# Performance work log

Hardware: AMD Instinct MI355X
Metric: run time of the kernel (lower is better)

## Reference

```python
import jax, jax.numpy as jnp
import numpy as np

NUM_HEADS = 8
FOCUSING_FACTOR = 3
EPS = 1e-6


def _focus(x, f):
    # focusing: x**f, renormalized to keep the original L2 norm per token
    n = jnp.linalg.norm(x, axis=-1, keepdims=True)
    xp = x ** f
    return xp / jnp.linalg.norm(xp, axis=-1, keepdims=True) * n


def _split_heads(x, h):
    # b n (h c) -> (b h) n c
    b, n, C = x.shape
    return x.reshape(b, n, h, C // h).transpose(0, 2, 1, 3).reshape(b * h, n, C // h)


def setup_inputs() -> dict:
    key = jax.random.key(0)
    ks = jax.random.split(key, 9)
    B, Nq, Nkv, C = 8, 4096, 4096, 512
    query = jax.random.normal(ks[0], (B, Nq, C), jnp.float32)
    key_in = jax.random.normal(ks[1], (B, Nkv, C), jnp.float32)
    value = jax.random.normal(ks[2], (B, Nkv, C), jnp.float32)
    Wq = jax.random.normal(ks[3], (C, C), jnp.float32) * 0.02
    Wk = jax.random.normal(ks[4], (C, C), jnp.float32) * 0.02
    Wv = jax.random.normal(ks[5], (C, C), jnp.float32) * 0.02
    Wp = jax.random.normal(ks[6], (C, C), jnp.float32) * 0.02
    bp = jnp.zeros((C,), jnp.float32)
    scale = jax.random.normal(ks[7], (1, 1, C), jnp.float32) * 0.02
    return {"query": query, "key_in": key_in, "value": value,
            "Wq": Wq, "Wk": Wk, "Wv": Wv, "Wp": Wp, "bp": bp,
            "scale": scale, "H": 64, "W": 64}


def reference(query, key_in, value, Wq, Wk, Wv, Wp, bp, scale, H, W):
    B, N, C = query.shape
    h = NUM_HEADS
    # projections (qkv_bias=False)
    q = jax.nn.relu(query @ Wq) + EPS
    k = jax.nn.relu(key_in @ Wk) + EPS
    v = value @ Wv
    s = jax.nn.softplus(scale)  # [1,1,C]
    q = q / s
    k = k / s
    q = _focus(q, FOCUSING_FACTOR)
    k = _focus(k, FOCUSING_FACTOR)
    q = _split_heads(q, h)  # [(B h), N, c]
    k = _split_heads(k, h)
    v = _split_heads(v, h)
    # z-normalizer: 1 / (q . sum_j k_j)
    z = 1.0 / (jnp.einsum('bic,bc->bi', q, k.sum(axis=1)) + EPS)
    # O(n) kv-aggregation path (i*j*(c+d) > c*d*(i+j) for these shapes)
    kv = jnp.einsum('bjc,bjd->bcd', k, v)
    x = jnp.einsum('bic,bcd,bi->bid', q, kv, z)
    # (b h) n c -> b n (h c)
    x = x.reshape(B, h, N, C // h).transpose(0, 2, 1, 3).reshape(B, N, C)
    # note: dwc(v) feature_map in the original is dead code (never added to x)
    return x @ Wp + bp
```

## Files before the change

kernel.cpp:

```cpp
#include <hip/hip_runtime.h>
#include <hip/hip_bf16.h>
#include <math.h>

typedef __attribute__((ext_vector_type(8))) short short8;
typedef __attribute__((ext_vector_type(4))) float f32x4;

#define MFMA16x16x32(A,B,C) __builtin_amdgcn_mfma_f32_16x16x32_bf16((A),(B),(C),0,0,0)
#define BAR_LGKM() do { asm volatile("s_waitcnt lgkmcnt(0)" ::: "memory"); \
                        __builtin_amdgcn_s_barrier(); } while (0)

__device__ __forceinline__ short f2b(float x) {
  __hip_bfloat16 h = __float2bfloat16(x);
  short s; __builtin_memcpy(&s, &h, 2); return s;
}
__device__ __forceinline__ float b2f(short s) {
  __hip_bfloat16 h; __builtin_memcpy(&h, &s, 2); return __bfloat162float(h);
}

__global__ __launch_bounds__(256)
void prep_kernel(const float* __restrict__ Wq, const float* __restrict__ Wk,
                 const float* __restrict__ Wv, const float* __restrict__ Wp,
                 const float* __restrict__ scale,
                 short* __restrict__ wpack, float* __restrict__ spls)
{
  const int b = blockIdx.x;
  const int t = threadIdx.x;
  if (b == 64) {
    for (int i = t; i < 512; i += 256) {
      float x = scale[i];
      spls[i] = (x > 20.f) ? x : log1pf(expf(x));
    }
    return;
  }
  const float* Ws[4] = {Wq, Wk, Wv, Wp};
  const int w = b >> 4, kf16 = b & 15;
  const float* W = Ws[w];
  short* dst = wpack + (size_t)w * (512 * 512);
  __shared__ short lds[32 * 512];
  for (int i = 0; i < 64; ++i) {
    int idx = i * 256 + t;
    int r = idx >> 9, c = idx & 511;
    lds[idx] = f2b(W[(size_t)(kf16 * 32 + r) * 512 + c]);
  }
  __syncthreads();
  for (int s = 0; s < 8; ++s) {
    int slot = s * 256 + t;
    int nf = slot >> 6, l = slot & 63;
    int n = nf * 16 + (l & 15);
    int k0 = 8 * (l >> 4);
    short8 v;
#pragma unroll
    for (int jj = 0; jj < 8; ++jj) v[jj] = lds[(k0 + jj) * 512 + n];
    *(short8*)(dst + ((size_t)(kf16 * 32 + nf) * 64 + l) * 8) = v;
  }
}

__global__ __launch_bounds__(512, 2)
void proj_kernel(const float* __restrict__ Aq, const float* __restrict__ Ak,
                 const float* __restrict__ Av, const short* __restrict__ Ax,
                 const short* __restrict__ wpack, const float* __restrict__ spls,
                 short* __restrict__ qf, short* __restrict__ kpk,
                 short* __restrict__ vpk, const float* __restrict__ bp,
                 float* __restrict__ outf, int mode_base)
{
  __shared__ char smem[65536];
  __shared__ float pnorm[2][8][64];
  __shared__ float facs[64];
  short* tile = (short*)smem;
  const int t = threadIdx.x;
  const int lane = t & 63;
  const int wid = t >> 6;
  const int g = lane >> 4;
  const int cl = lane & 15;
  const int bid = blockIdx.x;
  const int mode = (mode_base == 3) ? 3 : (bid % 3);
  const int rbi  = (mode_base == 3) ? bid : (bid / 3);
  const int rb = rbi << 6;
  const int sr = t >> 3;
  const int sc = t & 7;
  const int r1 = rbi & 3;
  const int r2 = (rbi >> 2) & 3;

  const float* Af = (mode == 0) ? Aq : (mode == 1) ? Ak : Av;
  const short8* wp8 = (const short8*)(wpack + (size_t)mode * (512 * 512));

  {
    char* dst = smem + sr * 272 + sc * 32;
    if (mode < 3) {
      const float* src = Af + (size_t)(rb + sr) * 512 + r1 * 128 + sc * 16;
      f32x4 a0 = *(const f32x4*)(src);
      f32x4 a1 = *(const f32x4*)(src + 4);
      f32x4 a2 = *(const f32x4*)(src + 8);
      f32x4 a3 = *(const f32x4*)(src + 12);
      short8 v0, v1;
#pragma unroll
      for (int j = 0; j < 4; ++j) {
        v0[j] = f2b(a0[j]); v0[4 + j] = f2b(a1[j]);
        v1[j] = f2b(a2[j]); v1[4 + j] = f2b(a3[j]);
      }
      *(short8*)dst = v0; *(short8*)(dst + 16) = v1;
    } else {
      const short* src = Ax + (size_t)(rb + sr) * 512 + r1 * 128 + sc * 16;
      *(short8*)dst = *(const short8*)src;
      *(short8*)(dst + 16) = *(const short8*)(src + 8);
    }
  }
  f32x4 zero4 = {0.f, 0.f, 0.f, 0.f};
  f32x4 acc[4][4];
#pragma unroll
  for (int rf = 0; rf < 4; ++rf)
#pragma unroll
    for (int cf = 0; cf < 4; ++cf) acc[rf][cf] = zero4;

  short8 bcur[4], bnxt[4];
  {
    const int kf0 = r1 * 4 + r2;
#pragma unroll
    for (int cf = 0; cf < 4; ++cf)
      bcur[cf] = wp8[((size_t)(kf0 * 32 + wid * 4 + cf)) * 64 + lane];
  }
  BAR_LGKM();

#pragma unroll
  for (int sl = 0; sl < 4; ++sl) {
    const int s_phys = (sl + r1) & 3;
    const int s_next = (s_phys + 1) & 3;
    char* cur = smem + (sl & 1) * 17408;
    f32x4 rA0, rA1, rA2, rA3;
    short8 rB0, rB1;
    if (sl < 3) {
      if (mode < 3) {
        const float* src = Af + (size_t)(rb + sr) * 512 + s_next * 128 + sc * 16;
        rA0 = *(const f32x4*)(src);
        rA1 = *(const f32x4*)(src + 4);
        rA2 = *(const f32x4*)(src + 8);
        rA3 = *(const f32x4*)(src + 12);
      } else {
        const short* src = Ax + (size_t)(rb + sr) * 512 + s_next * 128 + sc * 16;
        rB0 = *(const short8*)src;
        rB1 = *(const short8*)(src + 8);
      }
    }
#pragma unroll
    for (int kl = 0; kl < 4; ++kl) {
      const int k_phys = (kl + r2) & 3;
      const bool last = (sl == 3) && (kl == 3);
      if (!last) {
        const int kf_n = (kl < 3) ? (s_phys * 4 + ((kl + 1 + r2) & 3))
                                  : (((s_phys + 1) & 3) * 4 + r2);
#pragma unroll
        for (int cf = 0; cf < 4; ++cf)
          bnxt[cf] = wp8[((size_t)(kf_n * 32 + wid * 4 + cf)) * 64 + lane];
      }
      short8 af[4];
#pragma unroll
      for (int rf = 0; rf < 4; ++rf)
        af[rf] = *(const short8*)(cur + (rf * 16 + cl) * 272 + k_phys * 64 + 16 * g);
      __builtin_amdgcn_s_setprio(1);
#pragma unroll
      for (int rf = 0; rf < 4; ++rf)
#pragma unroll
        for (int cf = 0; cf < 4; ++cf)
          acc[rf][cf] = MFMA16x16x32(af[rf], bcur[cf], acc[rf][cf]);
      __builtin_amdgcn_s_setprio(0);
      if (!last) {
#pragma unroll
        for (int cf = 0; cf < 4; ++cf) bcur[cf] = bnxt[cf];
      }
    }
    if (sl < 3) {
      char* dst = smem + ((sl + 1) & 1) * 17408 + sr * 272 + sc * 32;
      short8 v0, v1;
      if (mode < 3) {
#pragma unroll
        for (int j = 0; j < 4; ++j) {
          v0[j] = f2b(rA0[j]); v0[4 + j] = f2b(rA1[j]);
          v1[j] = f2b(rA2[j]); v1[4 + j] = f2b(rA3[j]);
        }
      } else { v0 = rB0; v1 = rB1; }
      *(short8*)dst = v0; *(short8*)(dst + 16) = v1;
      BAR_LGKM();
    }
  }

  if (mode == 3) {
#pragma unroll
    for (int rf = 0; rf < 4; ++rf)
#pragma unroll
      for (int cf = 0; cf < 4; ++cf) {
        int c = wid * 64 + cf * 16 + cl;
        float bv = bp[c];
#pragma unroll
        for (int j = 0; j < 4; ++j)
          outf[(size_t)(rb + rf * 16 + 4 * g + j) * 512 + c] = acc[rf][cf][j] + bv;
      }
    return;
  }

  if (mode < 2) {
    float sp_inv[4];
#pragma unroll
    for (int cf = 0; cf < 4; ++cf) sp_inv[cf] = 1.f / spls[wid * 64 + cf * 16 + cl];
    float p2[4][4], p6[4][4];
#pragma unroll
    for (int rf = 0; rf < 4; ++rf)
#pragma unroll
      for (int j = 0; j < 4; ++j) { p2[rf][j] = 0.f; p6[rf][j] = 0.f; }
#pragma unroll
    for (int rf = 0; rf < 4; ++rf)
#pragma unroll
      for (int cf = 0; cf < 4; ++cf)
#pragma unroll
        for (int j = 0; j < 4; ++j) {
          float v = acc[rf][cf][j];
          v = fmaxf(v, 0.f) + 1e-6f;
          v *= sp_inv[cf];
          acc[rf][cf][j] = v;
          float v2 = v * v;
          p2[rf][j] += v2;
          p6[rf][j] += v2 * v2 * v2;
        }
#pragma unroll
    for (int m = 1; m < 16; m <<= 1) {
#pragma unroll
      for (int rf = 0; rf < 4; ++rf)
#pragma unroll
        for (int j = 0; j < 4; ++j) {
          p2[rf][j] += __shfl_xor(p2[rf][j], m, 64);
          p6[rf][j] += __shfl_xor(p6[rf][j], m, 64);
        }
    }
    if (cl == 0) {
#pragma unroll
      for (int rf = 0; rf < 4; ++rf)
#pragma unroll
        for (int j = 0; j < 4; ++j) {
          pnorm[0][wid][rf * 16 + 4 * g + j] = p2[rf][j];
          pnorm[1][wid][rf * 16 + 4 * g + j] = p6[rf][j];
        }
    }
    __syncthreads();
    if (t < 64) {
      float a = 0.f, b = 0.f;
#pragma unroll
      for (int w = 0; w < 8; ++w) { a += pnorm[0][w][t]; b += pnorm[1][w][t]; }
      facs[t] = sqrtf(a / b);
    }
    __syncthreads();
    float fac[4][4];
#pragma unroll
    for (int rf = 0; rf < 4; ++rf)
#pragma unroll
      for (int j = 0; j < 4; ++j) fac[rf][j] = facs[rf * 16 + 4 * g + j];
#pragma unroll
    for (int rf = 0; rf < 4; ++rf)
#pragma unroll
      for (int cf = 0; cf < 4; ++cf)
#pragma unroll
        for (int j = 0; j < 4; ++j) {
          float v = acc[rf][cf][j];
          float o = v * v * v * fac[rf][j];
          int r = rf * 16 + 4 * g + j;
          int c = wid * 64 + cf * 16 + cl;
          int byteoff = (r * 1024 + c * 2) ^ ((r & 7) << 4);
          *(short*)((char*)tile + byteoff) = f2b(o);
        }
  } else {
    __syncthreads();
#pragma unroll
    for (int rf = 0; rf < 4; ++rf)
#pragma unroll
      for (int cf = 0; cf < 4; ++cf)
#pragma unroll
        for (int j = 0; j < 4; ++j) {
          int r = rf * 16 + 4 * g + j;
          int c = wid * 64 + cf * 16 + cl;
          int byteoff = (r * 1024 + c * 2) ^ ((r & 7) << 4);
          *(short*)((char*)tile + byteoff) = f2b(acc[rf][cf][j]);
        }
  }
  __syncthreads();

  if (mode == 0) {
    const int r = t >> 3;
    const int c8 = t & 7;
#pragma unroll
    for (int s = 0; s < 8; ++s) {
      int ci = c8 + 8 * s;
      int byteoff = (r * 1024 + ci * 16) ^ ((r & 7) << 4);
      short8 v = *(const short8*)((const char*)tile + byteoff);
      *(short8*)(qf + (size_t)(rb + r) * 512 + ci * 8) = v;
    }
  } else {
    short* dstp = (mode == 1) ? kpk : vpk;
    const int l = lane;
    const int batch = rb >> 12;
    const int jf_base = (rb & 4095) >> 5;
#pragma unroll
    for (int s = 0; s < 8; ++s) {
      int fidx = wid * 8 + s;
      int jf = fidx >> 5;
      int cf = fidx & 31;
      int c = cf * 16 + (l & 15);
      int j0 = jf * 32 + 8 * (l >> 4);
      short8 v;
#pragma unroll
      for (int jj = 0; jj < 8; ++jj) {
        int j = j0 + jj;
        int byteoff = (j * 1024 + c * 2) ^ ((j & 7) << 4);
        v[jj] = *(const short*)((const char*)tile + byteoff);
      }
      int bh = batch * 8 + (cf >> 2);
      int cfh = cf & 3;
      int jfg = jf_base + jf;
      *(short8*)(dstp + (((size_t)(bh * 128 + jfg) * 4 + cfh) * 64 + l) * 8) = v;
    }
  }
}

__global__ __launch_bounds__(256)
void kv_kernel(const short* __restrict__ kpack, const short* __restrict__ vpack,
               float* __restrict__ pKV, float* __restrict__ pKS)
{
  __shared__ float red[4][64 * 64];
  __shared__ float ksacc[64];
  const int t = threadIdx.x;
  const int lane = t & 63;
  const int w = t >> 6;
  const int g = lane >> 4;
  const int cl = lane & 15;
  const int bh = blockIdx.x >> 3;
  const int sp = blockIdx.x & 7;
  if (t < 64) ksacc[t] = 0.f;
  __syncthreads();

  f32x4 zero4 = {0.f, 0.f, 0.f, 0.f};
  f32x4 acc[4][4];
#pragma unroll
  for (int df = 0; df < 4; ++df)
#pragma unroll
    for (int cf = 0; cf < 4; ++cf) acc[df][cf] = zero4;
  float ks[4] = {0.f, 0.f, 0.f, 0.f};
  const short8* kp = (const short8*)kpack;
  const short8* vp = (const short8*)vpack;

#pragma unroll
  for (int i = 0; i < 4; ++i) {
    int jfg = sp * 16 + w * 4 + i;
    size_t base = ((size_t)bh * 128 + jfg) * 4 * 64;
    short8 afr[4], bfr[4];
#pragma unroll
    for (int f = 0; f < 4; ++f) {
      afr[f] = vp[base + (size_t)f * 64 + lane];
      bfr[f] = kp[base + (size_t)f * 64 + lane];
    }
#pragma unroll
    for (int cf = 0; cf < 4; ++cf) {
      float s = 0.f;
#pragma unroll
      for (int jj = 0; jj < 8; ++jj) s += b2f(bfr[cf][jj]);
      ks[cf] += s;
    }
#pragma unroll
    for (int df = 0; df < 4; ++df)
#pragma unroll
      for (int cf = 0; cf < 4; ++cf)
        acc[df][cf] = MFMA16x16x32(afr[df], bfr[cf], acc[df][cf]);
  }

#pragma unroll
  for (int cf = 0; cf < 4; ++cf) {
    ks[cf] += __shfl_xor(ks[cf], 16, 64);
    ks[cf] += __shfl_xor(ks[cf], 32, 64);
  }
  if (lane < 16) {
#pragma unroll
    for (int cf = 0; cf < 4; ++cf) atomicAdd(&ksacc[cf * 16 + lane], ks[cf]);
  }

#pragma unroll
  for (int df = 0; df < 4; ++df)
#pragma unroll
    for (int cf = 0; cf < 4; ++cf)
#pragma unroll
      for (int j = 0; j < 4; ++j)
        red[w][(df * 16 + 4 * g + j) * 64 + cf * 16 + cl] = acc[df][cf][j];
  __syncthreads();

  float* dkv = pKV + (size_t)blockIdx.x * 4096;
  for (int i = t; i < 4096; i += 256)
    dkv[i] = red[0][i] + red[1][i] + red[2][i] + red[3][i];
  if (t < 64) pKS[(size_t)blockIdx.x * 64 + t] = ksacc[t];
}

__global__ __launch_bounds__(256)
void kv_reduce(const float* __restrict__ pKV, const float* __restrict__ pKS,
               short* __restrict__ kvT, float* __restrict__ ksum)
{
  const int bh = blockIdx.x;
  const int t = threadIdx.x;
  for (int i = t; i < 4096; i += 256) {
    float s = 0.f;
#pragma unroll
    for (int sp = 0; sp < 8; ++sp) s += pKV[(size_t)(bh * 8 + sp) * 4096 + i];
    kvT[(size_t)bh * 4096 + i] = f2b(s);
  }
  if (t < 64) {
    float s = 0.f;
#pragma unroll
    for (int sp = 0; sp < 8; ++sp) s += pKS[(size_t)(bh * 8 + sp) * 64 + t];
    ksum[bh * 64 + t] = s;
  }
}

__global__ __launch_bounds__(512)
void x_kernel(const short* __restrict__ qf, const short* __restrict__ kvT,
              const float* __restrict__ ksum, short* __restrict__ xout)
{
  __shared__ short xt[64 * 512];
  __shared__ float ksb[512];
  __shared__ float zb[64 * 8];
  const int t = threadIdx.x;
  const int lane = t & 63;
  const int wid = t >> 6;
  const int wr = wid >> 1;
  const int wc = wid & 1;
  const int g = lane >> 4;
  const int cl = lane & 15;
  const int rb = blockIdx.x << 6;
  const int batch = rb >> 12;

  ksb[t] = ksum[batch * 512 + t];
  __syncthreads();

  {
    int r = t >> 3, h = t & 7;
    const short8* qrow = (const short8*)(qf + (size_t)(rb + r) * 512 + h * 64);
    float d = 0.f;
#pragma unroll
    for (int c8 = 0; c8 < 8; ++c8) {
      short8 qv = qrow[c8];
#pragma unroll
      for (int jj = 0; jj < 8; ++jj) d += b2f(qv[jj]) * ksb[h * 64 + c8 * 8 + jj];
    }
    zb[r * 8 + h] = 1.f / (d + 1e-6f);
  }
  __syncthreads();

  f32x4 zero4 = {0.f, 0.f, 0.f, 0.f};
  f32x4 xacc[16];
#pragma unroll
  for (int i = 0; i < 16; ++i) xacc[i] = zero4;

  const short8* q8 = (const short8*)qf;
  const size_t qrowbase = (size_t)(rb + wr * 16 + cl) * 64;
#pragma unroll
  for (int hh = 0; hh < 4; ++hh) {
    int h = wc * 4 + hh;
    short8 af0 = q8[qrowbase + h * 8 + g];
    short8 af1 = q8[qrowbase + h * 8 + 4 + g];
    const short8* kv8 = (const short8*)kvT + ((size_t)(batch * 8 + h)) * 512;
#pragma unroll
    for (int nfl = 0; nfl < 4; ++nfl) {
      short8 b0 = kv8[(size_t)(nfl * 16 + cl) * 8 + g];
      short8 b1 = kv8[(size_t)(nfl * 16 + cl) * 8 + 4 + g];
      int nf = hh * 4 + nfl;
      xacc[nf] = MFMA16x16x32(af0, b0, xacc[nf]);
      xacc[nf] = MFMA16x16x32(af1, b1, xacc[nf]);
    }
  }
#pragma unroll
  for (int hh = 0; hh < 4; ++hh) {
    int h = wc * 4 + hh;
    float z4[4];
#pragma unroll
    for (int j = 0; j < 4; ++j) z4[j] = zb[(wr * 16 + 4 * g + j) * 8 + h];
#pragma unroll
    for (int nfl = 0; nfl < 4; ++nfl) {
      int nf = hh * 4 + nfl;
#pragma unroll
      for (int j = 0; j < 4; ++j) {
        float xv = xacc[nf][j] * z4[j];
        int r = wr * 16 + 4 * g + j;
        int c = wc * 256 + nf * 16 + cl;
        int byteoff = (r * 1024 + c * 2) ^ ((r & 7) << 4);
        *(short*)((char*)xt + byteoff) = f2b(xv);
      }
    }
  }
  __syncthreads();

  const int r = t >> 3;
  const int c8 = t & 7;
#pragma unroll
  for (int s = 0; s < 8; ++s) {
    int ci = c8 + 8 * s;
    int byteoff = (r * 1024 + ci * 16) ^ ((r & 7) << 4);
    short8 v = *(const short8*)((const char*)xt + byteoff);
    *(short8*)(xout + (size_t)(rb + r) * 512 + ci * 8) = v;
  }
}

extern "C" void kernel_launch(void* const* d_in, const int* in_sizes, int n_in,
                              void* d_out, int out_size, void* d_ws, size_t ws_size,
                              hipStream_t stream)
{
  const float* query  = (const float*)d_in[0];
  const float* key_in = (const float*)d_in[1];
  const float* value  = (const float*)d_in[2];
  const float* Wq     = (const float*)d_in[3];
  const float* Wk     = (const float*)d_in[4];
  const float* Wv     = (const float*)d_in[5];
  const float* Wp     = (const float*)d_in[6];
  const float* bp     = (const float*)d_in[7];
  const float* scale  = (const float*)d_in[8];
  float* out = (float*)d_out;

  char* ws = (char*)d_ws;
  size_t off = 0;
  auto alloc = [&](size_t bytes) -> void* {
    void* p = ws + off;
    off += (bytes + 255) & ~(size_t)255;
    return p;
  };
  float* spls  = (float*)alloc(512 * 4);
  short* wpack = (short*)alloc((size_t)4 * 512 * 512 * 2);
  short* qf    = (short*)alloc((size_t)32768 * 512 * 2);
  short* kpack = (short*)alloc((size_t)32768 * 512 * 2);
  short* vpack = (short*)alloc((size_t)32768 * 512 * 2);
  float* pKV   = (float*)alloc((size_t)512 * 4096 * 4);
  float* pKS   = (float*)alloc((size_t)512 * 64 * 4);
  short* kvT   = (short*)alloc((size_t)64 * 4096 * 2);
  float* ksum  = (float*)alloc((size_t)64 * 64 * 4);
  short* xbuf  = kpack;

  prep_kernel<<<65, 256, 0, stream>>>(Wq, Wk, Wv, Wp, scale, wpack, spls);
  proj_kernel<<<1536, 512, 0, stream>>>(query, key_in, value, nullptr, wpack, spls,
                                        qf, kpack, vpack, nullptr, nullptr, 0);
  kv_kernel<<<512, 256, 0, stream>>>(kpack, vpack, pKV, pKS);
  kv_reduce<<<64, 256, 0, stream>>>(pKV, pKS, kvT, ksum);
  x_kernel<<<512, 512, 0, stream>>>(qf, kvT, ksum, xbuf);
  proj_kernel<<<512, 512, 0, stream>>>(nullptr, nullptr, nullptr, xbuf, wpack, spls,
                                       nullptr, nullptr, nullptr, bp, out, 3);
}
```

Measured before the change: 199.4 us.

## Fuse kv-aggregation output and final projection into one kernel

Merges x_kernel and the mode-3 output projection into a single xout_kernel. The bf16 x tile stays in LDS and feeds the Wp GEMM directly, so it is no longer written to global memory and read back. This also removes one kernel launch and lets proj_kernel drop its mode-3 branches. The cost is that the fused kernel uses the full 64KB xt tile plus extra registers under launch_bounds(512,2), which may limit occupancy.

Result: faster. 186.6 us (-6.4%).

```diff
diff --git a/kernel.cpp b/kernel.cpp
--- a/kernel.cpp
+++ b/kernel.cpp
@@ -6,8 +6,8 @@
 typedef __attribute__((ext_vector_type(4))) float f32x4;
 
 #define MFMA16x16x32(A,B,C) __builtin_amdgcn_mfma_f32_16x16x32_bf16((A),(B),(C),0,0,0)
-#define BAR_LGKM() do { asm volatile("s_waitcnt lgkmcnt(0)" ::: "memory"); \
-                        __builtin_amdgcn_s_barrier(); } while (0)
+#define LGKM0()   asm volatile("s_waitcnt lgkmcnt(0)" ::: "memory")
+#define BAR_LGKM() do { LGKM0(); __builtin_amdgcn_s_barrier(); } while (0)
 
 __device__ __forceinline__ short f2b(float x) {
   __hip_bfloat16 h = __float2bfloat16(x);
@@ -57,11 +57,10 @@
 
 __global__ __launch_bounds__(512, 2)
 void proj_kernel(const float* __restrict__ Aq, const float* __restrict__ Ak,
-                 const float* __restrict__ Av, const short* __restrict__ Ax,
+                 const float* __restrict__ Av,
                  const short* __restrict__ wpack, const float* __restrict__ spls,
                  short* __restrict__ qf, short* __restrict__ kpk,
-                 short* __restrict__ vpk, const float* __restrict__ bp,
-                 float* __restrict__ outf, int mode_base)
+                 short* __restrict__ vpk)
 {
   __shared__ char smem[65536];
   __shared__ float pnorm[2][8][64];
@@ -73,8 +72,8 @@
   const int g = lane >> 4;
   const int cl = lane & 15;
   const int bid = blockIdx.x;
-  const int mode = (mode_base == 3) ? 3 : (bid % 3);
-  const int rbi  = (mode_base == 3) ? bid : (bid / 3);
+  const int mode = bid % 3;
+  const int rbi  = bid / 3;
   const int rb = rbi << 6;
   const int sr = t >> 3;
   const int sc = t & 7;
@@ -86,24 +85,18 @@
 
   {
     char* dst = smem + sr * 272 + sc * 32;
-    if (mode < 3) {
-      const float* src = Af + (size_t)(rb + sr) * 512 + r1 * 128 + sc * 16;
-      f32x4 a0 = *(const f32x4*)(src);
-      f32x4 a1 = *(const f32x4*)(src + 4);
-      f32x4 a2 = *(const f32x4*)(src + 8);
-      f32x4 a3 = *(const f32x4*)(src + 12);
-      short8 v0, v1;
-#pragma unroll
-      for (int j = 0; j < 4; ++j) {
-        v0[j] = f2b(a0[j]); v0[4 + j] = f2b(a1[j]);
-        v1[j] = f2b(a2[j]); v1[4 + j] = f2b(a3[j]);
-      }
-      *(short8*)dst = v0; *(short8*)(dst + 16) = v1;
-    } else {
-      const short* src = Ax + (size_t)(rb + sr) * 512 + r1 * 128 + sc * 16;
-      *(short8*)dst = *(const short8*)src;
-      *(short8*)(dst + 16) = *(const short8*)(src + 8);
-    }
+    const float* src = Af + (size_t)(rb + sr) * 512 + r1 * 128 + sc * 16;
+    f32x4 a0 = *(const f32x4*)(src);
+    f32x4 a1 = *(const f32x4*)(src + 4);
+    f32x4 a2 = *(const f32x4*)(src + 8);
+    f32x4 a3 = *(const f32x4*)(src + 12);
+    short8 v0, v1;
+#pragma unroll
+    for (int j = 0; j < 4; ++j) {
+      v0[j] = f2b(a0[j]); v0[4 + j] = f2b(a1[j]);
+      v1[j] = f2b(a2[j]); v1[4 + j] = f2b(a3[j]);
+    }
+    *(short8*)dst = v0; *(short8*)(dst + 16) = v1;
   }
   f32x4 zero4 = {0.f, 0.f, 0.f, 0.f};
   f32x4 acc[4][4];
@@ -127,19 +120,12 @@
     const int s_next = (s_phys + 1) & 3;
     char* cur = smem + (sl & 1) * 17408;
     f32x4 rA0, rA1, rA2, rA3;
-    short8 rB0, rB1;
     if (sl < 3) {
-      if (mode < 3) {
-        const float* src = Af + (size_t)(rb + sr) * 512 + s_next * 128 + sc * 16;
-        rA0 = *(const f32x4*)(src);
-        rA1 = *(const f32x4*)(src + 4);
-        rA2 = *(const f32x4*)(src + 8);
-        rA3 = *(const f32x4*)(src + 12);
-      } else {
-        const short* src = Ax + (size_t)(rb + sr) * 512 + s_next * 128 + sc * 16;
-        rB0 = *(const short8*)src;
-        rB1 = *(const short8*)(src + 8);
-      }
+      const float* src = Af + (size_t)(rb + sr) * 512 + s_next * 128 + sc * 16;
+      rA0 = *(const f32x4*)(src);
+      rA1 = *(const f32x4*)(src + 4);
+      rA2 = *(const f32x4*)(src + 8);
+      rA3 = *(const f32x4*)(src + 12);
     }
 #pragma unroll
     for (int kl = 0; kl < 4; ++kl) {
@@ -171,30 +157,14 @@
     if (sl < 3) {
       char* dst = smem + ((sl + 1) & 1) * 17408 + sr * 272 + sc * 32;
       short8 v0, v1;
-      if (mode < 3) {
-#pragma unroll
-        for (int j = 0; j < 4; ++j) {
-          v0[j] = f2b(rA0[j]); v0[4 + j] = f2b(rA1[j]);
-          v1[j] = f2b(rA2[j]); v1[4 + j] = f2b(rA3[j]);
-        }
-      } else { v0 = rB0; v1 = rB1; }
+#pragma unroll
+      for (int j = 0; j < 4; ++j) {
+        v0[j] = f2b(rA0[j]); v0[4 + j] = f2b(rA1[j]);
+        v1[j] = f2b(rA2[j]); v1[4 + j] = f2b(rA3[j]);
+      }
       *(short8*)dst = v0; *(short8*)(dst + 16) = v1;
       BAR_LGKM();
     }
-  }
-
-  if (mode == 3) {
-#pragma unroll
-    for (int rf = 0; rf < 4; ++rf)
-#pragma unroll
-      for (int cf = 0; cf < 4; ++cf) {
-        int c = wid * 64 + cf * 16 + cl;
-        float bv = bp[c];
-#pragma unroll
-        for (int j = 0; j < 4; ++j)
-          outf[(size_t)(rb + rf * 16 + 4 * g + j) * 512 + c] = acc[rf][cf][j] + bv;
-      }
-    return;
   }
 
   if (mode < 2) {
@@ -413,9 +383,10 @@
   }
 }
 
-__global__ __launch_bounds__(512)
-void x_kernel(const short* __restrict__ qf, const short* __restrict__ kvT,
-              const float* __restrict__ ksum, short* __restrict__ xout)
+__global__ __launch_bounds__(512, 2)
+void xout_kernel(const short* __restrict__ qf, const short* __restrict__ kvT,
+                 const float* __restrict__ ksum, const short* __restrict__ wpack,
+                 const float* __restrict__ bp, float* __restrict__ out)
 {
   __shared__ short xt[64 * 512];
   __shared__ float ksb[512];
@@ -427,8 +398,11 @@
   const int wc = wid & 1;
   const int g = lane >> 4;
   const int cl = lane & 15;
-  const int rb = blockIdx.x << 6;
+  const int bid = blockIdx.x;
+  const int rb = bid << 6;
   const int batch = rb >> 12;
+  const int r1 = bid & 3;
+  const int r2 = (bid >> 2) & 3;
 
   ksb[t] = ksum[batch * 512 + t];
   __syncthreads();
@@ -448,57 +422,110 @@
   __syncthreads();
 
   f32x4 zero4 = {0.f, 0.f, 0.f, 0.f};
-  f32x4 xacc[16];
-#pragma unroll
-  for (int i = 0; i < 16; ++i) xacc[i] = zero4;
-
-  const short8* q8 = (const short8*)qf;
-  const size_t qrowbase = (size_t)(rb + wr * 16 + cl) * 64;
-#pragma unroll
-  for (int hh = 0; hh < 4; ++hh) {
-    int h = wc * 4 + hh;
-    short8 af0 = q8[qrowbase + h * 8 + g];
-    short8 af1 = q8[qrowbase + h * 8 + 4 + g];
-    const short8* kv8 = (const short8*)kvT + ((size_t)(batch * 8 + h)) * 512;
-#pragma unroll
-    for (int nfl = 0; nfl < 4; ++nfl) {
-      short8 b0 = kv8[(size_t)(nfl * 16 + cl) * 8 + g];
-      short8 b1 = kv8[(size_t)(nfl * 16 + cl) * 8 + 4 + g];
-      int nf = hh * 4 + nfl;
-      xacc[nf] = MFMA16x16x32(af0, b0, xacc[nf]);
-      xacc[nf] = MFMA16x16x32(af1, b1, xacc[nf]);
-    }
-  }
-#pragma unroll
-  for (int hh = 0; hh < 4; ++hh) {
-    int h = wc * 4 + hh;
-    float z4[4];
-#pragma unroll
-    for (int j = 0; j < 4; ++j) z4[j] = zb[(wr * 16 + 4 * g + j) * 8 + h];
-#pragma unroll
-    for (int nfl = 0; nfl < 4; ++nfl) {
-      int nf = hh * 4 + nfl;
-#pragma unroll
-      for (int j = 0; j < 4; ++j) {
-        float xv = xacc[nf][j] * z4[j];
-        int r = wr * 16 + 4 * g + j;
-        int c = wc * 256 + nf * 16 + cl;
-        int byteoff = (r * 1024 + c * 2) ^ ((r & 7) << 4);
-        *(short*)((char*)xt + byteoff) = f2b(xv);
-      }
-    }
-  }
-  __syncthreads();
-
-  const int r = t >> 3;
-  const int c8 = t & 7;
-#pragma unroll
-  for (int s = 0; s < 8; ++s) {
-    int ci = c8 + 8 * s;
-    int byteoff = (r * 1024 + ci * 16) ^ ((r & 7) << 4);
-    short8 v = *(const short8*)((const char*)xt + byteoff);
-    *(short8*)(xout + (size_t)(rb + r) * 512 + ci * 8) = v;
-  }
+  {
+    f32x4 xacc[16];
+#pragma unroll
+    for (int i = 0; i < 16; ++i) xacc[i] = zero4;
+
+    const short8* q8 = (const short8*)qf;
+    const size_t qrowbase = (size_t)(rb + wr * 16 + cl) * 64;
+#pragma unroll
+    for (int hh = 0; hh < 4; ++hh) {
+      int h = wc * 4 + hh;
+      short8 af0 = q8[qrowbase + h * 8 + g];
+      short8 af1 = q8[qrowbase + h * 8 + 4 + g];
+      const short8* kv8 = (const short8*)kvT + ((size_t)(batch * 8 + h)) * 512;
+#pragma unroll
+      for (int nfl = 0; nfl < 4; ++nfl) {
+        short8 b0 = kv8[(size_t)(nfl * 16 + cl) * 8 + g];
+        short8 b1 = kv8[(size_t)(nfl * 16 + cl) * 8 + 4 + g];
+        int nf = hh * 4 + nfl;
+        xacc[nf] = MFMA16x16x32(af0, b0, xacc[nf]);
+        xacc[nf] = MFMA16x16x32(af1, b1, xacc[nf]);
+      }
+    }
+#pragma unroll
+    for (int hh = 0; hh < 4; ++hh) {
+      int h = wc * 4 + hh;
+      float z4[4];
+#pragma unroll
+      for (int j = 0; j < 4; ++j) z4[j] = zb[(wr * 16 + 4 * g + j) * 8 + h];
+#pragma unroll
+      for (int nfl = 0; nfl < 4; ++nfl) {
+        int nf = hh * 4 + nfl;
+#pragma unroll
+        for (int j = 0; j < 4; ++j) {
+          float xv = xacc[nf][j] * z4[j];
+          int r = wr * 16 + 4 * g + j;
+          int c = wc * 256 + nf * 16 + cl;
+          int byteoff = (r * 1024 + c * 2) ^ ((r & 7) << 4);
+          *(short*)((char*)xt + byteoff) = f2b(xv);
+        }
+      }
+    }
+  }
+  __syncthreads();
+
+  const short8* wp8 = (const short8*)(wpack + (size_t)3 * (512 * 512));
+  f32x4 acc[4][4];
+#pragma unroll
+  for (int rf = 0; rf < 4; ++rf)
+#pragma unroll
+    for (int cf = 0; cf < 4; ++cf) acc[rf][cf] = zero4;
+
+  short8 bcur[4], bnxt[4];
+  {
+    const int kf0 = r1 * 4 + r2;
+#pragma unroll
+    for (int cf = 0; cf < 4; ++cf)
+      bcur[cf] = wp8[((size_t)(kf0 * 32 + wid * 4 + cf)) * 64 + lane];
+  }
+#pragma unroll
+  for (int sl = 0; sl < 4; ++sl) {
+    const int s_phys = (sl + r1) & 3;
+#pragma unroll
+    for (int kl = 0; kl < 4; ++kl) {
+      const int k_phys = (kl + r2) & 3;
+      const int kf = s_phys * 4 + k_phys;
+      const bool last = (sl == 3) && (kl == 3);
+      if (!last) {
+        const int kf_n = (kl < 3) ? (s_phys * 4 + ((kl + 1 + r2) & 3))
+                                  : (((s_phys + 1) & 3) * 4 + r2);
+#pragma unroll
+        for (int cf = 0; cf < 4; ++cf)
+          bnxt[cf] = wp8[((size_t)(kf_n * 32 + wid * 4 + cf)) * 64 + lane];
+      }
+      short8 af[4];
+#pragma unroll
+      for (int rf = 0; rf < 4; ++rf) {
+        int row = rf * 16 + cl;
+        int byteoff = (row * 1024 + (kf * 32 + 8 * g) * 2) ^ ((row & 7) << 4);
+        af[rf] = *(const short8*)((const char*)xt + byteoff);
+      }
+      __builtin_amdgcn_s_setprio(1);
+#pragma unroll
+      for (int rf = 0; rf < 4; ++rf)
+#pragma unroll
+        for (int cf = 0; cf < 4; ++cf)
+          acc[rf][cf] = MFMA16x16x32(af[rf], bcur[cf], acc[rf][cf]);
+      __builtin_amdgcn_s_setprio(0);
+      if (!last) {
+#pragma unroll
+        for (int cf = 0; cf < 4; ++cf) bcur[cf] = bnxt[cf];
+      }
+    }
+  }
+
+#pragma unroll
+  for (int rf = 0; rf < 4; ++rf)
+#pragma unroll
+    for (int cf = 0; cf < 4; ++cf) {
+      int c = wid * 64 + cf * 16 + cl;
+      float bv = bp[c];
+#pragma unroll
+      for (int j = 0; j < 4; ++j)
+        out[(size_t)(rb + rf * 16 + 4 * g + j) * 512 + c] = acc[rf][cf][j] + bv;
+    }
 }
 
 extern "C" void kernel_launch(void* const* d_in, const int* in_sizes, int n_in,
@@ -532,14 +559,11 @@
   float* pKS   = (float*)alloc((size_t)512 * 64 * 4);
   short* kvT   = (short*)alloc((size_t)64 * 4096 * 2);
   float* ksum  = (float*)alloc((size_t)64 * 64 * 4);
-  short* xbuf  = kpack;
 
   prep_kernel<<<65, 256, 0, stream>>>(Wq, Wk, Wv, Wp, scale, wpack, spls);
-  proj_kernel<<<1536, 512, 0, stream>>>(query, key_in, value, nullptr, wpack, spls,
-                                        qf, kpack, vpack, nullptr, nullptr, 0);
+  proj_kernel<<<1536, 512, 0, stream>>>(query, key_in, value, wpack, spls,
+                                        qf, kpack, vpack);
   kv_kernel<<<512, 256, 0, stream>>>(kpack, vpack, pKV, pKS);
   kv_reduce<<<64, 256, 0, stream>>>(pKV, pKS, kvT, ksum);
-  x_kernel<<<512, 512, 0, stream>>>(qf, kvT, ksum, xbuf);
-  proj_kernel<<<512, 512, 0, stream>>>(nullptr, nullptr, nullptr, xbuf, wpack, spls,
-                                       nullptr, nullptr, nullptr, bp, out, 3);
-}
+  xout_kernel<<<512, 512, 0, stream>>>(qf, kvT, ksum, wpack, bp, out);
+}
```
